# Performance work log

Measured on AMD Instinct MI355X. Metric: run time of the kernel, lower is better.

Reference implementation:

```python
import jax, jax.numpy as jnp
import numpy as np

NUM_EXPERTS = 8
TOP_K = 2
HIDDEN = 512
INTERMEDIATE = 2048
BATCH, SEQ = 8, 2048


def setup_inputs() -> dict:
    key = jax.random.key(0)
    ks = jax.random.split(key, 7)
    s_in = 1.0 / np.sqrt(HIDDEN)
    s_mid = 1.0 / np.sqrt(INTERMEDIATE)
    return {
        "x": jax.random.normal(ks[0], (BATCH, SEQ, HIDDEN), jnp.float32),
        "Wg": jax.random.normal(ks[1], (HIDDEN, NUM_EXPERTS), jnp.float32) * s_in,
        "bg": jnp.zeros((NUM_EXPERTS,), jnp.float32),
        "W1": jax.random.normal(ks[2], (NUM_EXPERTS, HIDDEN, INTERMEDIATE), jnp.float32) * s_in,
        "b1": jnp.zeros((NUM_EXPERTS, INTERMEDIATE), jnp.float32),
        "W2": jax.random.normal(ks[3], (NUM_EXPERTS, INTERMEDIATE, HIDDEN), jnp.float32) * s_mid,
        "b2": jnp.zeros((NUM_EXPERTS, HIDDEN), jnp.float32),
    }


def reference(x, Wg, bg, W1, b1, W2, b2):
    B, S, H = x.shape
    xf = x.reshape(B * S, H)  # flatten tokens, as in call()

    # Linear gating: full softmax probabilities over experts [T, E]
    logits = xf @ Wg + bg
    probs = jax.nn.softmax(logits, axis=-1)
    # Top-k routing indices (expert_indices in the original)
    _, top_idx = jax.lax.top_k(probs, TOP_K)  # [T, k]
    # Token->expert mask: any(expert_indices == e), matching top_k>1 branch
    mask = jnp.any(top_idx[:, :, None] == jnp.arange(NUM_EXPERTS)[None, None, :], axis=1)  # [T, E] bool

    # Combine weight per token/expert: raw softmax prob (NOT renormalized),
    # exactly expert_weights[:, expert_id] gated by the routing mask.
    comb = probs * mask.astype(probs.dtype)  # [T, E]

    out = jnp.zeros_like(xf)
    for e in range(NUM_EXPERTS):  # small fixed expert count
        h = jax.nn.gelu(xf @ W1[e] + b1[e])  # [T, F]
        y = h @ W2[e] + b2[e]                # [T, H]
        out = out + comb[:, e:e + 1] * y
    return out.reshape(B, S, H)
```

## Files before the change

kernel.cpp:

```cpp
#include <hip/hip_runtime.h>
#include <stdint.h>

typedef unsigned short u16;
typedef unsigned int   u32;
typedef short  s8v  __attribute__((ext_vector_type(8)));
typedef __bf16 bf8v __attribute__((ext_vector_type(8)));
typedef float  f4v  __attribute__((ext_vector_type(4)));
typedef u16    u16x4 __attribute__((ext_vector_type(4)));
typedef u16    u16x8 __attribute__((ext_vector_type(8)));

#define NTOK   16384
#define HD     512
#define FD     2048
#define NE     8
#define MAXROWS 33280
#define MAXTILES 520
#define FCH    32
#define NCH    64

#define CTRL_OFF   0
#define TOKE_OFF   8192
#define COMB_OFF   73728
#define LIST_OFF   598016
#define ROWW_OFF   731136
#define XBF_OFF    1048576
#define W1T_OFF    17825792
#define W2T_OFF    34603008
#define WS_NEED    51380224ull

__device__ __forceinline__ u16 f2bf(float f) {
    union { float f; u32 u; } v; v.f = f;
    u32 r = v.u + 0x7FFFu + ((v.u >> 16) & 1u);
    return (u16)(r >> 16);
}
__device__ __forceinline__ float gelu_f(float v) {
    float u = 0.7978845608028654f * (v + 0.044715f * v * v * v);
    float t = 1.f - 2.f / (__expf(2.f * u) + 1.f);
    return 0.5f * v * (1.f + t);
}

template <typename V>
__device__ __forceinline__ auto mfma_try(V a, V b, f4v c, int)
    -> decltype(__builtin_amdgcn_mfma_f32_16x16x32_bf16(a, b, c, 0, 0, 0)) {
    return __builtin_amdgcn_mfma_f32_16x16x32_bf16(a, b, c, 0, 0, 0);
}
template <typename V>
__device__ __forceinline__ f4v mfma_try(V a, V b, f4v c, long) {
    return __builtin_amdgcn_mfma_f32_16x16x32_bf16(
        __builtin_bit_cast(bf8v, a), __builtin_bit_cast(bf8v, b), c, 0, 0, 0);
}
__device__ __forceinline__ f4v mfma16(s8v a, s8v b, f4v c) { return mfma_try(a, b, c, 0); }

__device__ __forceinline__ void gload16(const u16* g, u16* l) {
    __builtin_amdgcn_global_load_lds(
        (const __attribute__((address_space(1))) unsigned int*)g,
        (__attribute__((address_space(3))) unsigned int*)l, 16, 0, 0);
}

__global__ __launch_bounds__(256) void k_fallback(float* __restrict__ out) {
    int i = (blockIdx.x * 256 + threadIdx.x) * 4;
    *(f4v*)(out + i) = (f4v){0.f, 0.f, 0.f, 0.f};
}

__global__ __launch_bounds__(256) void k_zero(int* __restrict__ ctrl, int* __restrict__ list,
                                              float* __restrict__ roww, float* __restrict__ out) {
    int id = blockIdx.x * 256 + threadIdx.x;
    *(f4v*)(out + (size_t)id * 4) = (f4v){0.f, 0.f, 0.f, 0.f};
    if (id < MAXROWS) { list[id] = 0; roww[id] = 0.f; }
    if (id < 64) ctrl[id] = 0;
}

__global__ __launch_bounds__(256) void k_transpose(const float* __restrict__ in, u16* __restrict__ out,
                                                   int R, int C) {
    __shared__ float tile[64][65];
    size_t base = (size_t)blockIdx.z * R * C;
    const float* ip = in + base;
    u16* op = out + base;
    int c0 = blockIdx.x * 64, r0 = blockIdx.y * 64;
#pragma unroll
    for (int i = 0; i < 4; i++) {
        int idx = threadIdx.x + i * 256;
        int r = idx >> 4, c4 = (idx & 15) * 4;
        f4v v = *(const f4v*)(ip + (size_t)(r0 + r) * C + c0 + c4);
#pragma unroll
        for (int j = 0; j < 4; j++) tile[r][c4 + j] = v[j];
    }
    __syncthreads();
#pragma unroll
    for (int i = 0; i < 4; i++) {
        int idx = threadIdx.x + i * 256;
        int c = idx >> 4, r4 = (idx & 15) * 4;
        u16x4 o;
#pragma unroll
        for (int j = 0; j < 4; j++) o[j] = f2bf(tile[r4 + j][c]);
        *(u16x4*)(op + (size_t)(c0 + c) * R + r0 + r4) = o;
    }
}

__global__ __launch_bounds__(256) void k_gate(const float* __restrict__ x, const float* __restrict__ Wg,
                                              const float* __restrict__ bg, float* __restrict__ comb,
                                              int* __restrict__ toke, u16* __restrict__ xbf) {
    int lane = threadIdx.x & 63;
    int t = (blockIdx.x * 4 + (threadIdx.x >> 6)) & (NTOK - 1);
    const float* xr = x + (size_t)t * HD;
    f4v xa = *(const f4v*)(xr + lane * 8);
    f4v xb = *(const f4v*)(xr + lane * 8 + 4);
    u16x8 o;
#pragma unroll
    for (int j = 0; j < 4; j++) { o[j] = f2bf(xa[j]); o[4 + j] = f2bf(xb[j]); }
    *(u16x8*)(xbf + (size_t)t * HD + lane * 8) = o;

    float p[8];
#pragma unroll
    for (int e = 0; e < 8; e++) p[e] = 0.f;
#pragma unroll
    for (int j = 0; j < 4; j++) {
        int h0 = lane * 8 + j, h1 = lane * 8 + 4 + j;
        f4v wa0 = *(const f4v*)(Wg + h0 * 8);
        f4v wa1 = *(const f4v*)(Wg + h0 * 8 + 4);
        f4v wb0 = *(const f4v*)(Wg + h1 * 8);
        f4v wb1 = *(const f4v*)(Wg + h1 * 8 + 4);
#pragma unroll
        for (int e = 0; e < 4; e++) {
            p[e]     += xa[j] * wa0[e] + xb[j] * wb0[e];
            p[4 + e] += xa[j] * wa1[e] + xb[j] * wb1[e];
        }
    }
#pragma unroll
    for (int off = 32; off > 0; off >>= 1)
#pragma unroll
        for (int e = 0; e < 8; e++) p[e] += __shfl_xor(p[e], off, 64);
#pragma unroll
    for (int e = 0; e < 8; e++) p[e] += bg[e];
    float mx = p[0];
#pragma unroll
    for (int e = 1; e < 8; e++) mx = fmaxf(mx, p[e]);
    float pr[8]; float s = 0.f;
#pragma unroll
    for (int e = 0; e < 8; e++) { pr[e] = __expf(p[e] - mx); s += pr[e]; }
    float inv = 1.f / s;
#pragma unroll
    for (int e = 0; e < 8; e++) pr[e] *= inv;
    int i1 = 0; float v1 = pr[0];
#pragma unroll
    for (int e = 1; e < 8; e++) if (pr[e] > v1) { v1 = pr[e]; i1 = e; }
    int i2 = 0; float v2 = -1.f;
#pragma unroll
    for (int e = 0; e < 8; e++) if (e != i1 && pr[e] > v2) { v2 = pr[e]; i2 = e; }
    if (lane == 0) {
#pragma unroll
        for (int e = 0; e < 8; e++) comb[t * 8 + e] = (e == i1 || e == i2) ? pr[e] : 0.f;
        toke[t] = i1 | (i2 << 8);
    }
}

__global__ __launch_bounds__(1024) void k_count(const int* __restrict__ toke, int* __restrict__ ctrl) {
    __shared__ int sCnt[8];
    if (threadIdx.x < 8) sCnt[threadIdx.x] = 0;
    __syncthreads();
    int t = blockIdx.x * 1024 + threadIdx.x;
    int te = toke[t];
    atomicAdd(&sCnt[te & 7], 1);
    atomicAdd(&sCnt[(te >> 8) & 7], 1);
    __syncthreads();
    if (threadIdx.x < 8) atomicAdd(&ctrl[threadIdx.x], sCnt[threadIdx.x]);
}

__global__ __launch_bounds__(640) void k_plan(int* __restrict__ ctrl) {
    __shared__ int sOff[9], sSeg[9];
    if (threadIdx.x == 0) {
        int seg = 0, tt = 0;
        for (int e = 0; e < 8; e++) {
            sSeg[e] = seg; sOff[e] = tt;
            ctrl[16 + e] = seg;
            int nt = (ctrl[e] + 63) >> 6;
            tt += nt; seg += nt * 64;
        }
        sOff[8] = tt; sSeg[8] = seg;
        ctrl[24] = seg;
        ctrl[25] = (tt < MAXTILES) ? tt : MAXTILES;
    }
    __syncthreads();
    int ntile = sOff[8] < MAXTILES ? sOff[8] : MAXTILES;
    for (int tt = threadIdx.x; tt < ntile; tt += 640) {
        int e = 0;
        while (e < 7 && tt >= sOff[e + 1]) e++;
        int i = tt - sOff[e];
        ctrl[32 + tt * 3]     = e;
        ctrl[32 + tt * 3 + 1] = sSeg[e] + i * 64;
        ctrl[32 + tt * 3 + 2] = i * 64;
    }
}

__global__ __launch_bounds__(1024) void k_scatter(const int* __restrict__ toke, const float* __restrict__ comb,
                                                  int* __restrict__ ctrl, int* __restrict__ list,
                                                  float* __restrict__ roww) {
    __shared__ int sCnt[8], sBase[8];
    if (threadIdx.x < 8) sCnt[threadIdx.x] = 0;
    __syncthreads();
    int t = blockIdx.x * 1024 + threadIdx.x;
    int te = toke[t];
    int e1 = te & 7, e2 = (te >> 8) & 7;
    int r1 = atomicAdd(&sCnt[e1], 1);
    int r2 = atomicAdd(&sCnt[e2], 1);
    __syncthreads();
    if (threadIdx.x < 8) sBase[threadIdx.x] = atomicAdd(&ctrl[8 + threadIdx.x], sCnt[threadIdx.x]);
    __syncthreads();
    int g1 = min(ctrl[16 + e1] + sBase[e1] + r1, MAXROWS - 1);
    list[g1] = t; roww[g1] = comb[t * 8 + e1];
    int g2 = min(ctrl[16 + e2] + sBase[e2] + r2, MAXROWS - 1);
    list[g2] = t; roww[g2] = comb[t * 8 + e2];
}

__global__ __launch_bounds__(512, 4) void k_main(const u16* __restrict__ xbf, const float* __restrict__ b1g,
                                                 const float* __restrict__ b2g, const u16* __restrict__ W1T,
                                                 const u16* __restrict__ W2T, const int* __restrict__ ctrl,
                                                 int* __restrict__ steal, const int* __restrict__ list,
                                                 const float* __restrict__ roww, float* __restrict__ out) {
    __shared__ u16 sW1[32 * 512];
    __shared__ u16 sW2[512 * 32];
    __shared__ u16 sH[64 * 40];
    __shared__ int sTile;
    const int tid = threadIdx.x, wave = tid >> 6, lane = tid & 63;
    const int quad = lane >> 4, l15 = lane & 15;
    const int m4 = wave & 3, f2 = wave >> 2;
    const int fs = f2 * 16 + l15;
    const int total = min(ctrl[25], MAXTILES);

    const int w2n  = ((wave * 64 + lane) >> 2);
    const int w2cu = lane & 3;

    for (;;) {
        if (tid == 0) sTile = atomicAdd(steal, 1);
        __syncthreads();
        int bt = sTile;
        if (bt >= total) break;
        int e      = ctrl[32 + bt * 3] & 7;
        int row0   = min(ctrl[32 + bt * 3 + 1], MAXROWS - 64);
        int inseg0 = ctrl[32 + bt * 3 + 2];
        int cnt    = ctrl[e];
        const u16* w1e = W1T + (size_t)e * FD * HD;
        const u16* w2e = W2T + (size_t)e * HD * FD;
        const float* b1e = b1g + e * FD;

        int mA = m4 * 16 + l15;
        int tokA = (inseg0 + mA < cnt) ? (list[row0 + mA] & (NTOK - 1)) : 0;
        const u16* xrow = xbf + (size_t)tokA * HD + quad * 8;

        f4v Y[4][4];
#pragma unroll
        for (int mb = 0; mb < 4; mb++)
#pragma unroll
            for (int nb = 0; nb < 4; nb++) Y[mb][nb] = (f4v){0.f, 0.f, 0.f, 0.f};

#define STAGE_W1(CC) {                                                              \
        const u16* wb = w1e + (size_t)(CC) * FCH * HD;                              \
        _Pragma("unroll")                                                           \
        for (int t8 = 0; t8 < 4; t8++) {                                            \
            int f = t8 * 8 + wave;                                                  \
            int g = (lane & ~7) | ((lane & 7) ^ (f & 7));                           \
            gload16(wb + (size_t)f * HD + g * 8, sW1 + f * 512);                    \
        } }
#define STAGE_W2(CC) {                                                              \
        const u16* wb = w2e + (size_t)(CC) * FCH;                                   \
        _Pragma("unroll")                                                           \
        for (int t8 = 0; t8 < 4; t8++) {                                            \
            int n = t8 * 128 + w2n;                                                 \
            int g = w2cu ^ ((n >> 2) & 3);                                          \
            gload16(wb + (size_t)n * FD + g * 8, sW2 + (t8 * 512 + wave * 64) * 8); \
        } }

        STAGE_W1(0);
        STAGE_W2(0);
        __syncthreads();

        for (int c = 0; c < NCH; c++) {
            f4v h = (f4v){0.f, 0.f, 0.f, 0.f};
#pragma unroll
            for (int ks = 0; ks < 16; ks++) {
                s8v a = *(const s8v*)(xrow + ks * 32);
                int cidx = ks * 4 + quad;
                int phys = (cidx & ~7) | ((cidx & 7) ^ (fs & 7));
                s8v b = *(const s8v*)(sW1 + fs * 512 + phys * 8);
                h = mfma16(a, b, h);
            }
            float bb = b1e[c * FCH + fs];
#pragma unroll
            for (int r = 0; r < 4; r++)
                sH[(m4 * 16 + quad * 4 + r) * 40 + fs] = f2bf(gelu_f(h[r] + bb));
            asm volatile("s_waitcnt vmcnt(0) lgkmcnt(0)" ::: "memory");
            __builtin_amdgcn_s_barrier();
            __builtin_amdgcn_sched_barrier(0);
            if (c + 1 < NCH) STAGE_W1(c + 1);
            s8v aH[4];
#pragma unroll
            for (int mb = 0; mb < 4; mb++)
                aH[mb] = *(const s8v*)(sH + (mb * 16 + l15) * 40 + quad * 8);
#pragma unroll
            for (int nb = 0; nb < 4; nb++) {
                int n = wave * 64 + nb * 16 + l15;
                s8v bw = *(const s8v*)(sW2 + n * 32 + ((quad ^ ((n >> 2) & 3)) * 8));
#pragma unroll
                for (int mb = 0; mb < 4; mb++) Y[mb][nb] = mfma16(aH[mb], bw, Y[mb][nb]);
            }
            asm volatile("s_waitcnt lgkmcnt(0)" ::: "memory");
            __builtin_amdgcn_s_barrier();
            __builtin_amdgcn_sched_barrier(0);
            if (c + 1 < NCH) STAGE_W2(c + 1);
            asm volatile("s_waitcnt vmcnt(4)" ::: "memory");
            __builtin_amdgcn_s_barrier();
            __builtin_amdgcn_sched_barrier(0);
        }
        float b2v[4];
#pragma unroll
        for (int nb = 0; nb < 4; nb++) b2v[nb] = b2g[e * HD + wave * 64 + nb * 16 + l15];
#pragma unroll
        for (int mb = 0; mb < 4; mb++) {
#pragma unroll
            for (int r = 0; r < 4; r++) {
                int m = mb * 16 + quad * 4 + r;
                bool val = (inseg0 + m) < cnt;
                int tok = list[row0 + m] & (NTOK - 1);
                float wgt = val ? roww[row0 + m] : 0.f;
                float* orow = out + (size_t)tok * HD + wave * 64 + l15;
#pragma unroll
                for (int nb = 0; nb < 4; nb++)
                    atomicAdd(orow + nb * 16, (Y[mb][nb][r] + b2v[nb]) * wgt);
            }
        }
#undef STAGE_W1
#undef STAGE_W2
    }
}

extern "C" void kernel_launch(void* const* d_in, const int* in_sizes, int n_in,
                              void* d_out, int out_size, void* d_ws, size_t ws_size,
                              hipStream_t stream) {
    const float* x  = (const float*)d_in[0];
    const float* Wg = (const float*)d_in[1];
    const float* bg = (const float*)d_in[2];
    const float* W1 = (const float*)d_in[3];
    const float* b1 = (const float*)d_in[4];
    const float* W2 = (const float*)d_in[5];
    const float* b2 = (const float*)d_in[6];
    (void)in_sizes; (void)n_in; (void)out_size;
    float* out = (float*)d_out;

    if (ws_size < WS_NEED) {
        k_fallback<<<(NTOK * HD / 4) / 256, 256, 0, stream>>>(out);
        return;
    }

    char* ws = (char*)d_ws;
    int*   ctrl = (int*)(ws + CTRL_OFF);
    int*   toke = (int*)(ws + TOKE_OFF);
    float* comb = (float*)(ws + COMB_OFF);
    int*   list = (int*)(ws + LIST_OFF);
    float* roww = (float*)(ws + ROWW_OFF);
    u16*   xbf  = (u16*)(ws + XBF_OFF);
    u16*   w1t  = (u16*)(ws + W1T_OFF);
    u16*   w2t  = (u16*)(ws + W2T_OFF);

    k_zero<<<(NTOK * HD / 4) / 256, 256, 0, stream>>>(ctrl, list, roww, out);
    k_transpose<<<dim3(FD / 64, HD / 64, NE), dim3(256), 0, stream>>>(W1, w1t, HD, FD);
    k_transpose<<<dim3(HD / 64, FD / 64, NE), dim3(256), 0, stream>>>(W2, w2t, FD, HD);
    k_gate<<<NTOK / 4, 256, 0, stream>>>(x, Wg, bg, comb, toke, xbf);
    k_count<<<NTOK / 1024, 1024, 0, stream>>>(toke, ctrl);
    k_plan<<<1, 640, 0, stream>>>(ctrl);
    k_scatter<<<NTOK / 1024, 1024, 0, stream>>>(toke, comb, ctrl, list, roww);
    k_main<<<512, 512, 0, stream>>>(xbf, b1, b2, w1t, w2t, ctrl, ctrl + 26, list, roww, out);
}
```

Measured before the change: 916.5 us.

## Double MoE tile to 128 rows with 1024-thread blocks and chunked W2 layout

Raises the per-task row tile from 64 to 128 tokens and uses 16 waves per block, so each staged W1/W2 chunk in LDS is reused across twice as many tokens. This roughly halves weight traffic per token. W2 is re-laid out into contiguous 32-column chunks during the transpose so each stage reads one contiguous block. The x fragments are also hoisted into registers once per task instead of being reloaded every chunk. The trade-offs are higher register pressure (A[16] plus Y[8][2]), fewer tasks for load balance, and more padding rows in partially filled tiles.

```diff
diff --git a/kernel.cpp b/kernel.cpp
--- a/kernel.cpp
+++ b/kernel.cpp
@@ -13,8 +13,8 @@
 #define HD     512
 #define FD     2048
 #define NE     8
-#define MAXROWS 33280
-#define MAXTILES 520
+#define MAXROWS 33792
+#define MAXTASK 272
 #define FCH    32
 #define NCH    64
 
@@ -22,7 +22,7 @@
 #define TOKE_OFF   8192
 #define COMB_OFF   73728
 #define LIST_OFF   598016
-#define ROWW_OFF   731136
+#define ROWW_OFF   733184
 #define XBF_OFF    1048576
 #define W1T_OFF    17825792
 #define W2T_OFF    34603008
@@ -71,7 +71,7 @@
 }
 
 __global__ __launch_bounds__(256) void k_transpose(const float* __restrict__ in, u16* __restrict__ out,
-                                                   int R, int C) {
+                                                   int R, int C, int mode) {
     __shared__ float tile[64][65];
     size_t base = (size_t)blockIdx.z * R * C;
     const float* ip = in + base;
@@ -93,7 +93,12 @@
         u16x4 o;
 #pragma unroll
         for (int j = 0; j < 4; j++) o[j] = f2bf(tile[r4 + j][c]);
-        *(u16x4*)(op + (size_t)(c0 + c) * R + r0 + r4) = o;
+        if (mode == 0) {
+            *(u16x4*)(op + (size_t)(c0 + c) * R + r0 + r4) = o;
+        } else {
+            int f = r0 + r4, n = c0 + c;
+            *(u16x4*)(op + (size_t)(f >> 5) * (C * 32) + (size_t)n * 32 + (f & 31)) = o;
+        }
     }
 }
 
@@ -167,28 +172,25 @@
 }
 
 __global__ __launch_bounds__(640) void k_plan(int* __restrict__ ctrl) {
-    __shared__ int sOff[9], sSeg[9];
+    __shared__ int sOff[9];
     if (threadIdx.x == 0) {
         int seg = 0, tt = 0;
         for (int e = 0; e < 8; e++) {
-            sSeg[e] = seg; sOff[e] = tt;
+            sOff[e] = tt;
             ctrl[16 + e] = seg;
-            int nt = (ctrl[e] + 63) >> 6;
-            tt += nt; seg += nt * 64;
-        }
-        sOff[8] = tt; sSeg[8] = seg;
+            int nt = (ctrl[e] + 127) >> 7;
+            tt += nt; seg += nt * 128;
+        }
+        sOff[8] = tt;
         ctrl[24] = seg;
-        ctrl[25] = (tt < MAXTILES) ? tt : MAXTILES;
-    }
-    __syncthreads();
-    int ntile = sOff[8] < MAXTILES ? sOff[8] : MAXTILES;
-    for (int tt = threadIdx.x; tt < ntile; tt += 640) {
+        ctrl[25] = (tt < MAXTASK) ? tt : MAXTASK;
+    }
+    __syncthreads();
+    int ntask = sOff[8] < MAXTASK ? sOff[8] : MAXTASK;
+    for (int t = threadIdx.x; t < ntask; t += 640) {
         int e = 0;
-        while (e < 7 && tt >= sOff[e + 1]) e++;
-        int i = tt - sOff[e];
-        ctrl[32 + tt * 3]     = e;
-        ctrl[32 + tt * 3 + 1] = sSeg[e] + i * 64;
-        ctrl[32 + tt * 3 + 2] = i * 64;
+        while (e < 7 && t >= sOff[e + 1]) e++;
+        ctrl[64 + t] = e | ((t - sOff[e]) << 4);
     }
 }
 
@@ -212,62 +214,65 @@
     list[g2] = t; roww[g2] = comb[t * 8 + e2];
 }
 
-__global__ __launch_bounds__(512, 4) void k_main(const u16* __restrict__ xbf, const float* __restrict__ b1g,
-                                                 const float* __restrict__ b2g, const u16* __restrict__ W1T,
-                                                 const u16* __restrict__ W2T, const int* __restrict__ ctrl,
-                                                 int* __restrict__ steal, const int* __restrict__ list,
-                                                 const float* __restrict__ roww, float* __restrict__ out) {
+__global__ __launch_bounds__(1024, 4) void k_main(const u16* __restrict__ xbf, const float* __restrict__ b1g,
+                                                  const float* __restrict__ b2g, const u16* __restrict__ W1T,
+                                                  const u16* __restrict__ W2C, const int* __restrict__ ctrl,
+                                                  int* __restrict__ steal, const int* __restrict__ list,
+                                                  const float* __restrict__ roww, float* __restrict__ out) {
     __shared__ u16 sW1[32 * 512];
     __shared__ u16 sW2[512 * 32];
-    __shared__ u16 sH[64 * 40];
+    __shared__ u16 sH[128 * 40];
     __shared__ int sTile;
     const int tid = threadIdx.x, wave = tid >> 6, lane = tid & 63;
     const int quad = lane >> 4, l15 = lane & 15;
-    const int m4 = wave & 3, f2 = wave >> 2;
-    const int fs = f2 * 16 + l15;
-    const int total = min(ctrl[25], MAXTILES);
-
-    const int w2n  = ((wave * 64 + lane) >> 2);
-    const int w2cu = lane & 3;
+    const int m8 = wave & 7, fb = wave >> 3;
+    const int fs = fb * 16 + l15;
+    const int total = min(ctrl[25], MAXTASK);
 
     for (;;) {
         if (tid == 0) sTile = atomicAdd(steal, 1);
         __syncthreads();
         int bt = sTile;
         if (bt >= total) break;
-        int e      = ctrl[32 + bt * 3] & 7;
-        int row0   = min(ctrl[32 + bt * 3 + 1], MAXROWS - 64);
-        int inseg0 = ctrl[32 + bt * 3 + 2];
+        int mword = ctrl[64 + bt];
+        int e  = mword & 7;
+        int it = mword >> 4;
+        int row0   = min(ctrl[16 + e] + it * 128, MAXROWS - 128);
+        int inseg0 = it * 128;
         int cnt    = ctrl[e];
         const u16* w1e = W1T + (size_t)e * FD * HD;
-        const u16* w2e = W2T + (size_t)e * HD * FD;
+        const u16* w2e = W2C + (size_t)e * HD * FD;
         const float* b1e = b1g + e * FD;
 
-        int mA = m4 * 16 + l15;
+        int mA = m8 * 16 + l15;
         int tokA = (inseg0 + mA < cnt) ? (list[row0 + mA] & (NTOK - 1)) : 0;
         const u16* xrow = xbf + (size_t)tokA * HD + quad * 8;
-
-        f4v Y[4][4];
-#pragma unroll
-        for (int mb = 0; mb < 4; mb++)
-#pragma unroll
-            for (int nb = 0; nb < 4; nb++) Y[mb][nb] = (f4v){0.f, 0.f, 0.f, 0.f};
+        s8v A[16];
+#pragma unroll
+        for (int ks = 0; ks < 16; ks++) A[ks] = *(const s8v*)(xrow + ks * 32);
+
+        f4v Y[8][2];
+#pragma unroll
+        for (int mb = 0; mb < 8; mb++)
+#pragma unroll
+            for (int nb = 0; nb < 2; nb++) Y[mb][nb] = (f4v){0.f, 0.f, 0.f, 0.f};
 
 #define STAGE_W1(CC) {                                                              \
         const u16* wb = w1e + (size_t)(CC) * FCH * HD;                              \
         _Pragma("unroll")                                                           \
-        for (int t8 = 0; t8 < 4; t8++) {                                            \
-            int f = t8 * 8 + wave;                                                  \
+        for (int t8 = 0; t8 < 2; t8++) {                                            \
+            int f = t8 * 16 + wave;                                                 \
             int g = (lane & ~7) | ((lane & 7) ^ (f & 7));                           \
             gload16(wb + (size_t)f * HD + g * 8, sW1 + f * 512);                    \
         } }
 #define STAGE_W2(CC) {                                                              \
-        const u16* wb = w2e + (size_t)(CC) * FCH;                                   \
+        const u16* wb = w2e + (size_t)(CC) * (HD * FCH);                            \
         _Pragma("unroll")                                                           \
-        for (int t8 = 0; t8 < 4; t8++) {                                            \
-            int n = t8 * 128 + w2n;                                                 \
-            int g = w2cu ^ ((n >> 2) & 3);                                          \
-            gload16(wb + (size_t)n * FD + g * 8, sW2 + (t8 * 512 + wave * 64) * 8); \
+        for (int t8 = 0; t8 < 2; t8++) {                                            \
+            int bn = t8 * 256 + wave * 16;                                          \
+            int n = bn + (lane >> 2);                                               \
+            int g = (lane & 3) ^ ((n >> 2) & 3);                                    \
+            gload16(wb + (size_t)n * 32 + g * 8, sW2 + bn * 32);                    \
         } }
 
         STAGE_W1(0);
@@ -278,53 +283,52 @@
             f4v h = (f4v){0.f, 0.f, 0.f, 0.f};
 #pragma unroll
             for (int ks = 0; ks < 16; ks++) {
-                s8v a = *(const s8v*)(xrow + ks * 32);
                 int cidx = ks * 4 + quad;
                 int phys = (cidx & ~7) | ((cidx & 7) ^ (fs & 7));
                 s8v b = *(const s8v*)(sW1 + fs * 512 + phys * 8);
-                h = mfma16(a, b, h);
+                h = mfma16(A[ks], b, h);
             }
             float bb = b1e[c * FCH + fs];
 #pragma unroll
             for (int r = 0; r < 4; r++)
-                sH[(m4 * 16 + quad * 4 + r) * 40 + fs] = f2bf(gelu_f(h[r] + bb));
+                sH[(m8 * 16 + quad * 4 + r) * 40 + fs] = f2bf(gelu_f(h[r] + bb));
             asm volatile("s_waitcnt vmcnt(0) lgkmcnt(0)" ::: "memory");
             __builtin_amdgcn_s_barrier();
             __builtin_amdgcn_sched_barrier(0);
             if (c + 1 < NCH) STAGE_W1(c + 1);
-            s8v aH[4];
-#pragma unroll
-            for (int mb = 0; mb < 4; mb++)
+            s8v aH[8];
+#pragma unroll
+            for (int mb = 0; mb < 8; mb++)
                 aH[mb] = *(const s8v*)(sH + (mb * 16 + l15) * 40 + quad * 8);
 #pragma unroll
-            for (int nb = 0; nb < 4; nb++) {
-                int n = wave * 64 + nb * 16 + l15;
+            for (int nb = 0; nb < 2; nb++) {
+                int n = wave * 32 + nb * 16 + l15;
                 s8v bw = *(const s8v*)(sW2 + n * 32 + ((quad ^ ((n >> 2) & 3)) * 8));
 #pragma unroll
-                for (int mb = 0; mb < 4; mb++) Y[mb][nb] = mfma16(aH[mb], bw, Y[mb][nb]);
+                for (int mb = 0; mb < 8; mb++) Y[mb][nb] = mfma16(aH[mb], bw, Y[mb][nb]);
             }
             asm volatile("s_waitcnt lgkmcnt(0)" ::: "memory");
             __builtin_amdgcn_s_barrier();
             __builtin_amdgcn_sched_barrier(0);
             if (c + 1 < NCH) STAGE_W2(c + 1);
-            asm volatile("s_waitcnt vmcnt(4)" ::: "memory");
+            asm volatile("s_waitcnt vmcnt(2)" ::: "memory");
             __builtin_amdgcn_s_barrier();
             __builtin_amdgcn_sched_barrier(0);
         }
-        float b2v[4];
-#pragma unroll
-        for (int nb = 0; nb < 4; nb++) b2v[nb] = b2g[e * HD + wave * 64 + nb * 16 + l15];
-#pragma unroll
-        for (int mb = 0; mb < 4; mb++) {
+        float b2v[2];
+#pragma unroll
+        for (int nb = 0; nb < 2; nb++) b2v[nb] = b2g[e * HD + wave * 32 + nb * 16 + l15];
+#pragma unroll
+        for (int mb = 0; mb < 8; mb++) {
 #pragma unroll
             for (int r = 0; r < 4; r++) {
                 int m = mb * 16 + quad * 4 + r;
                 bool val = (inseg0 + m) < cnt;
                 int tok = list[row0 + m] & (NTOK - 1);
                 float wgt = val ? roww[row0 + m] : 0.f;
-                float* orow = out + (size_t)tok * HD + wave * 64 + l15;
-#pragma unroll
-                for (int nb = 0; nb < 4; nb++)
+                float* orow = out + (size_t)tok * HD + wave * 32 + l15;
+#pragma unroll
+                for (int nb = 0; nb < 2; nb++)
                     atomicAdd(orow + nb * 16, (Y[mb][nb][r] + b2v[nb]) * wgt);
             }
         }
@@ -359,14 +363,14 @@
     float* roww = (float*)(ws + ROWW_OFF);
     u16*   xbf  = (u16*)(ws + XBF_OFF);
     u16*   w1t  = (u16*)(ws + W1T_OFF);
-    u16*   w2t  = (u16*)(ws + W2T_OFF);
+    u16*   w2c  = (u16*)(ws + W2T_OFF);
 
     k_zero<<<(NTOK * HD / 4) / 256, 256, 0, stream>>>(ctrl, list, roww, out);
-    k_transpose<<<dim3(FD / 64, HD / 64, NE), dim3(256), 0, stream>>>(W1, w1t, HD, FD);
-    k_transpose<<<dim3(HD / 64, FD / 64, NE), dim3(256), 0, stream>>>(W2, w2t, FD, HD);
+    k_transpose<<<dim3(FD / 64, HD / 64, NE), dim3(256), 0, stream>>>(W1, w1t, HD, FD, 0);
+    k_transpose<<<dim3(HD / 64, FD / 64, NE), dim3(256), 0, stream>>>(W2, w2c, FD, HD, 1);
     k_gate<<<NTOK / 4, 256, 0, stream>>>(x, Wg, bg, comb, toke, xbf);
     k_count<<<NTOK / 1024, 1024, 0, stream>>>(toke, ctrl);
     k_plan<<<1, 640, 0, stream>>>(ctrl);
     k_scatter<<<NTOK / 1024, 1024, 0, stream>>>(toke, comb, ctrl, list, roww);
-    k_main<<<512, 512, 0, stream>>>(xbf, b1, b2, w1t, w2t, ctrl, ctrl + 26, list, roww, out);
-}
+    k_main<<<256, 1024, 0, stream>>>(xbf, b1, b2, w1t, w2c, ctrl, ctrl + 26, list, roww, out);
+}
```

Result: slower. 1.336 ms (+45.8%).
